# Optimization experiments

Measured on AMD Instinct MI355X. Metric: run time of the kernel, lower is better.

## Reference

```python
import jax, jax.numpy as jnp
import numpy as np

B = 32768
HID = 512          # hidden_dim
DIM = 256          # output dim
MAX_N = 17         # max_n + 1
KEY_MID = (MAX_N + HID) // 2   # 264
DEC_MID = (HID + DIM) // 2     # 384
SP_MID = (HID + MAX_N) // 2    # 264


def _linear_params(k, fan_in, fan_out):
    k1, k2 = jax.random.split(k)
    lim = 1.0 / np.sqrt(fan_in)
    W = jax.random.uniform(k1, (fan_in, fan_out), minval=-lim, maxval=lim, dtype=jnp.float32)
    b = jax.random.uniform(k2, (fan_out,), minval=-lim, maxval=lim, dtype=jnp.float32)
    return W, b


def setup_inputs() -> dict:
    key = jax.random.key(0)
    ks = jax.random.split(key, 7)
    z = jax.random.normal(ks[0], (B, HID), dtype=jnp.float32)
    key_W1, key_b1 = _linear_params(ks[1], MAX_N, KEY_MID)
    key_W2, key_b2 = _linear_params(ks[2], KEY_MID, HID)
    dec_W1, dec_b1 = _linear_params(ks[3], HID, DEC_MID)
    dec_W2, dec_b2 = _linear_params(ks[4], DEC_MID, DIM)
    sp_W1, sp_b1 = _linear_params(ks[5], HID, SP_MID)
    sp_W2, sp_b2 = _linear_params(ks[6], SP_MID, MAX_N)
    return dict(
        z=z,
        key_W1=key_W1, key_b1=key_b1,
        key_g1=jnp.ones((KEY_MID,), jnp.float32), key_be1=jnp.zeros((KEY_MID,), jnp.float32),
        key_W2=key_W2, key_b2=key_b2,
        dec_W1=dec_W1, dec_b1=dec_b1, dec_W2=dec_W2, dec_b2=dec_b2,
        sp_W1=sp_W1, sp_b1=sp_b1,
        sp_g1=jnp.ones((SP_MID,), jnp.float32), sp_be1=jnp.zeros((SP_MID,), jnp.float32),
        sp_W2=sp_W2, sp_b2=sp_b2,
    )


def _ln(x, g, b):
    m = x.mean(-1, keepdims=True)
    v = x.var(-1, keepdims=True)
    return (x - m) / jnp.sqrt(v + 1e-5) * g + b


def _ragged_indices(n):
    # n: np.int array [B]; returns batch ids and within-sample positions k
    n = np.asarray(n)
    batch = np.repeat(np.arange(n.shape[0]), n)
    starts = np.concatenate([np.zeros(1, dtype=np.int64), np.cumsum(n)[:-1]])
    k = np.arange(batch.shape[0]) - starts[batch]
    return batch, k


def reference(z, key_W1, key_b1, key_g1, key_be1, key_W2, key_b2,
              dec_W1, dec_b1, dec_W2, dec_b2,
              sp_W1, sp_b1, sp_g1, sp_be1, sp_W2, sp_b2):
    # size_pred MLP: Linear -> LayerNorm -> ReLU -> Linear
    h = jax.nn.relu(_ln(z @ sp_W1 + sp_b1, sp_g1, sp_be1))
    n_pred = h @ sp_W2 + sp_b2                       # [B, MAX_N]
    n = np.asarray(jnp.argmax(n_pred, axis=-1))      # concrete sizes (ragged)
    batch_np, k_np = _ragged_indices(n)
    batch = jnp.asarray(batch_np)
    k = jnp.asarray(k_np)
    pos = jax.nn.one_hot(k, MAX_N, dtype=jnp.float32)            # [T, MAX_N]
    # key_net: Linear -> LayerNorm -> ReLU -> Linear
    keys = jax.nn.relu(_ln(pos @ key_W1 + key_b1, key_g1, key_be1)) @ key_W2 + key_b2  # [T, HID]
    vals_rep = z[batch]                              # repeat_interleave via gather
    zp = vals_rep * keys
    # decoder: Linear -> ReLU -> Linear (no layernorm by default)
    x = jax.nn.relu(zp @ dec_W1 + dec_b1) @ dec_W2 + dec_b2      # [T, DIM]
    return x, batch
```

## Files before the change

### kernel.cpp

```cpp
#include <hip/hip_runtime.h>
#include <hip/hip_bf16.h>

#define B_N   32768
#define HID   512
#define DIM   256
#define MAXN  17
#define SM    264
#define DM    384

typedef __attribute__((ext_vector_type(8))) short bf16x8;
typedef __attribute__((ext_vector_type(4))) float f32x4;

static __device__ __forceinline__ unsigned short f2bf(float x) {
  union { float f; unsigned u; } v; v.f = x;
  unsigned r = (v.u + 0x7FFFu + ((v.u >> 16) & 1u)) >> 16;
  return (unsigned short)r;
}

static __device__ __forceinline__ unsigned pkbf(float a, float b) {
  __hip_bfloat162 h = __float22bfloat162_rn(float2{a, b});
  union { __hip_bfloat162 h; unsigned u; } cv; cv.h = h;
  return cv.u;
}

__global__ __launch_bounds__(320, 3) void sizepred_kernel(
    const float* __restrict__ z,  const float* __restrict__ W1,
    const float* __restrict__ b1, const float* __restrict__ g1,
    const float* __restrict__ be1, const float* __restrict__ W2,
    const float* __restrict__ b2, int* __restrict__ n_out)
{
  __shared__ __align__(16) char smem[33024 + 2 * 16896];
  float* zs   = (float*)smem;
  float* us   = (float*)smem;
  float* wch0 = (float*)(smem + 33024);
  float* wch1 = (float*)(smem + 33024 + 16896);
  __shared__ float lnm[16], lnr[16];
  __shared__ float log17[16 * 17];

  const int tid = threadIdx.x;
  const int b0  = blockIdx.x * 16;

  const bool act = tid < 264;
  const int  s0  = (tid / 66) * 4;
  const int  j0  = (tid % 66) * 4;

  float acc[4][4];
#pragma unroll
  for (int i = 0; i < 4; ++i)
#pragma unroll
    for (int q = 0; q < 4; ++q) acc[i][q] = 0.f;

  float4 nz0, nz1, nz2, nz3;
  if (act) {
    const float4* wsrc = (const float4*)W1;
    nz0 = wsrc[0 * 264 + tid];
    nz1 = wsrc[1 * 264 + tid];
    nz2 = wsrc[2 * 264 + tid];
    nz3 = wsrc[3 * 264 + tid];
  }
  for (int idx = tid; idx < 2048; idx += 320) {
    int r = idx >> 7, c4 = idx & 127;
    float4 v = ((const float4*)z)[(size_t)(b0 + r) * 128 + c4];
    *(float4*)&zs[r * 516 + c4 * 4] = v;
  }
  if (act) {
    float4* wd = (float4*)wch0;
    wd[0 * 264 + tid] = nz0;
    wd[1 * 264 + tid] = nz1;
    wd[2 * 264 + tid] = nz2;
    wd[3 * 264 + tid] = nz3;
  }
  __syncthreads();

#pragma unroll 1
  for (int ch = 0; ch < 32; ++ch) {
    const float* cw = (ch & 1) ? wch1 : wch0;
    float*       nw = (ch & 1) ? wch0 : wch1;
    if (act && ch + 1 < 32) {
      const float4* wsrc = (const float4*)(W1 + (size_t)(ch + 1) * 16 * 264);
      nz0 = wsrc[0 * 264 + tid];
      nz1 = wsrc[1 * 264 + tid];
      nz2 = wsrc[2 * 264 + tid];
      nz3 = wsrc[3 * 264 + tid];
    }
    if (act) {
      const int zb = ch * 16;
#pragma unroll
      for (int u = 0; u < 4; ++u) {
        float4 za0 = *(const float4*)&zs[(s0 + 0) * 516 + zb + u * 4];
        float4 za1 = *(const float4*)&zs[(s0 + 1) * 516 + zb + u * 4];
        float4 za2 = *(const float4*)&zs[(s0 + 2) * 516 + zb + u * 4];
        float4 za3 = *(const float4*)&zs[(s0 + 3) * 516 + zb + u * 4];
#pragma unroll
        for (int e = 0; e < 4; ++e) {
          float4 w = *(const float4*)&cw[(u * 4 + e) * 264 + j0];
          float a0 = (e == 0) ? za0.x : (e == 1) ? za0.y : (e == 2) ? za0.z : za0.w;
          float a1 = (e == 0) ? za1.x : (e == 1) ? za1.y : (e == 2) ? za1.z : za1.w;
          float a2 = (e == 0) ? za2.x : (e == 1) ? za2.y : (e == 2) ? za2.z : za2.w;
          float a3 = (e == 0) ? za3.x : (e == 1) ? za3.y : (e == 2) ? za3.z : za3.w;
          acc[0][0] += a0 * w.x; acc[0][1] += a0 * w.y; acc[0][2] += a0 * w.z; acc[0][3] += a0 * w.w;
          acc[1][0] += a1 * w.x; acc[1][1] += a1 * w.y; acc[1][2] += a1 * w.z; acc[1][3] += a1 * w.w;
          acc[2][0] += a2 * w.x; acc[2][1] += a2 * w.y; acc[2][2] += a2 * w.z; acc[2][3] += a2 * w.w;
          acc[3][0] += a3 * w.x; acc[3][1] += a3 * w.y; acc[3][2] += a3 * w.z; acc[3][3] += a3 * w.w;
        }
      }
      if (ch + 1 < 32) {
        float4* wd = (float4*)nw;
        wd[0 * 264 + tid] = nz0;
        wd[1 * 264 + tid] = nz1;
        wd[2 * 264 + tid] = nz2;
        wd[3 * 264 + tid] = nz3;
      }
    }
    __syncthreads();
  }

  float4 o0, o1, o2, o3;
  if (act) {
    float4 bb = *(const float4*)&b1[j0];
    o0.x = acc[0][0] + bb.x; o0.y = acc[0][1] + bb.y; o0.z = acc[0][2] + bb.z; o0.w = acc[0][3] + bb.w;
    o1.x = acc[1][0] + bb.x; o1.y = acc[1][1] + bb.y; o1.z = acc[1][2] + bb.z; o1.w = acc[1][3] + bb.w;
    o2.x = acc[2][0] + bb.x; o2.y = acc[2][1] + bb.y; o2.z = acc[2][2] + bb.z; o2.w = acc[2][3] + bb.w;
    o3.x = acc[3][0] + bb.x; o3.y = acc[3][1] + bb.y; o3.z = acc[3][2] + bb.z; o3.w = acc[3][3] + bb.w;
  }
  __syncthreads();
  if (act) {
    *(float4*)&us[(s0 + 0) * 268 + j0] = o0;
    *(float4*)&us[(s0 + 1) * 268 + j0] = o1;
    *(float4*)&us[(s0 + 2) * 268 + j0] = o2;
    *(float4*)&us[(s0 + 3) * 268 + j0] = o3;
  }
  __syncthreads();

  if (tid < 16) {
    float s = 0.f, q = 0.f;
    for (int j = 0; j < 264; ++j) { float v = us[tid * 268 + j]; s += v; q += v * v; }
    float m   = s / 264.f;
    float var = q / 264.f - m * m;
    lnm[tid] = m;
    lnr[tid] = 1.f / sqrtf(var + 1e-5f);
  }
  __syncthreads();

  for (int idx = tid; idx < 16 * 264; idx += 320) {
    int s = idx / 264, j = idx - s * 264;
    float v = (us[s * 268 + j] - lnm[s]) * lnr[s] * g1[j] + be1[j];
    us[s * 268 + j] = fmaxf(v, 0.f);
  }
  __syncthreads();

  if (tid < 272) {
    int s = tid / 17, jj = tid - s * 17;
    float a = b2[jj];
    const float* up = &us[s * 268];
#pragma unroll 4
    for (int c = 0; c < 264; c += 4) {
      float4 u = *(const float4*)(up + c);
      a += u.x * W2[(c + 0) * 17 + jj];
      a += u.y * W2[(c + 1) * 17 + jj];
      a += u.z * W2[(c + 2) * 17 + jj];
      a += u.w * W2[(c + 3) * 17 + jj];
    }
    log17[tid] = a;
  }
  __syncthreads();

  if (tid < 16) {
    int best = 0; float bv = log17[tid * 17];
    for (int jj = 1; jj < 17; ++jj) {
      float v = log17[tid * 17 + jj];
      if (v > bv) { bv = v; best = jj; }
    }
    n_out[b0 + tid] = best;
  }
}

__global__ __launch_bounds__(1024) void scan_kernel(const int* __restrict__ n,
                                                    int* __restrict__ starts)
{
  __shared__ int part[1024];
  const int tid  = threadIdx.x;
  const int base = tid * 32;
  int loc[32];
  int s = 0;
#pragma unroll
  for (int i = 0; i < 8; ++i) {
    int4 v = ((const int4*)(n + base))[i];
    loc[i * 4 + 0] = v.x; loc[i * 4 + 1] = v.y;
    loc[i * 4 + 2] = v.z; loc[i * 4 + 3] = v.w;
    s += v.x + v.y + v.z + v.w;
  }
  part[tid] = s;
  __syncthreads();
  for (int off = 1; off < 1024; off <<= 1) {
    int v   = part[tid];
    int add = (tid >= off) ? part[tid - off] : 0;
    __syncthreads();
    part[tid] = v + add;
    __syncthreads();
  }
  int run = part[tid] - s;
#pragma unroll
  for (int i = 0; i < 8; ++i) {
    int4 w;
    w.x = run; run += loc[i * 4 + 0];
    w.y = run; run += loc[i * 4 + 1];
    w.z = run; run += loc[i * 4 + 2];
    w.w = run; run += loc[i * 4 + 3];
    ((int4*)(starts + base))[i] = w;
  }
  if (tid == 1023) starts[B_N] = run;
}

__global__ __launch_bounds__(256) void scatter_kernel(
    const int* __restrict__ n, const int* __restrict__ starts,
    int* __restrict__ bi, int* __restrict__ ki, float* __restrict__ out, int T)
{
  int b = blockIdx.x * 256 + threadIdx.x;
  if (b >= B_N) return;
  int st = starts[b], nn = n[b];
  float* ob = out + (size_t)T * DIM;
  for (int k = 0; k < nn; ++k) {
    bi[st + k] = b;
    ki[st + k] = k;
    ob[st + k] = (float)b;
  }
}

__global__ __launch_bounds__(320) void keys_kernel(
    const float* __restrict__ W1, const float* __restrict__ b1,
    const float* __restrict__ g1, const float* __restrict__ be1,
    const float* __restrict__ W2, const float* __restrict__ b2,
    float* __restrict__ ktab)
{
  __shared__ float hs[264];
  __shared__ float mr[2];
  const int kk = blockIdx.x, tid = threadIdx.x;
  if (tid < 264) hs[tid] = W1[kk * 264 + tid] + b1[tid];
  __syncthreads();
  if (tid == 0) {
    float s = 0.f, q = 0.f;
    for (int j = 0; j < 264; ++j) { float v = hs[j]; s += v; q += v * v; }
    float m = s / 264.f;
    mr[0] = m;
    mr[1] = 1.f / sqrtf(q / 264.f - m * m + 1e-5f);
  }
  __syncthreads();
  if (tid < 264) hs[tid] = fmaxf((hs[tid] - mr[0]) * mr[1] * g1[tid] + be1[tid], 0.f);
  __syncthreads();
  for (int c = tid; c < 512; c += 320) {
    float a = b2[c];
    for (int j = 0; j < 264; ++j) a += hs[j] * W2[j * 512 + c];
    ktab[kk * 512 + c] = a;
  }
}

__global__ __launch_bounds__(64) void pack_kernel(
    const float* __restrict__ W1, const float* __restrict__ W2,
    short* __restrict__ W1p, short* __restrict__ W2p)
{
  const int g = blockIdx.x, l = threadIdx.x;
  const float* W; int nt, kt, N;
  if (g < 384) { W = W1; kt = g / 24; nt = g % 24; N = 384; }
  else         { W = W2; int gg = g - 384; kt = gg / 16; nt = gg % 16; N = 256; }
  const int krow = kt * 32 + ((l >> 4) << 3);
  const int col  = nt * 16 + (l & 15);
  short v[8];
#pragma unroll
  for (int j = 0; j < 8; ++j)
    v[j] = (short)f2bf(W[(size_t)(krow + j) * N + col]);
  short* d = (g < 384) ? (W1p + ((size_t)g * 64 + l) * 8)
                       : (W2p + ((size_t)(g - 384) * 64 + l) * 8);
  *(bf16x8*)d = *(bf16x8*)v;
}

__global__ __launch_bounds__(256, 4) void decoder_kernel(
    const float* __restrict__ z,  const float* __restrict__ ktab,
    const short* __restrict__ W1p, const float* __restrict__ b1,
    const short* __restrict__ W2p, const float* __restrict__ b2,
    const int* __restrict__ bi,   const int* __restrict__ ki,
    float* __restrict__ out, int T)
{
  __shared__ __align__(16) short zps[16384];
  __shared__ int tb[32], tk[32];

  const int tid  = threadIdx.x;
  const int wave = tid >> 6;
  const int lane = tid & 63;
  const int t0   = blockIdx.x * 32;

  if (tid < 32) {
    int t = t0 + tid;
    tb[tid] = (t < T) ? bi[t] : 0;
    tk[tid] = (t < T) ? ki[t] : 0;
  }
  __syncthreads();

#pragma unroll
  for (int it = 0; it < 8; ++it) {
    int chunk = tid + it * 256;
    int l  = chunk & 63;
    int mt = (chunk >> 6) & 1;
    int kt = chunk >> 7;
    int m  = mt * 16 + (l & 15);
    int k0 = kt * 32 + ((l >> 4) << 3);
    const float4* zr = (const float4*)(z    + (size_t)tb[m] * 512 + k0);
    const float4* kr = (const float4*)(ktab + (size_t)tk[m] * 512 + k0);
    float4 z0 = zr[0], z1 = zr[1], k4 = kr[0], k5 = kr[1];
    uint4 u;
    u.x = pkbf(z0.x * k4.x, z0.y * k4.y);
    u.y = pkbf(z0.z * k4.z, z0.w * k4.w);
    u.z = pkbf(z1.x * k5.x, z1.y * k5.y);
    u.w = pkbf(z1.z * k5.z, z1.w * k5.w);
    *(uint4*)&zps[(size_t)chunk * 8] = u;
  }
  __syncthreads();

  f32x4 acc[2][6];
#pragma unroll
  for (int mt = 0; mt < 2; ++mt)
#pragma unroll
    for (int j = 0; j < 6; ++j) acc[mt][j] = (f32x4){0.f, 0.f, 0.f, 0.f};

  {
    const short* wb = W1p + ((size_t)(wave * 6) * 64 + lane) * 8;
#pragma unroll 4
    for (int kt = 0; kt < 16; ++kt) {
      bf16x8 a0 = *(bf16x8*)&zps[((kt * 2 + 0) * 64 + lane) * 8];
      bf16x8 a1 = *(bf16x8*)&zps[((kt * 2 + 1) * 64 + lane) * 8];
#pragma unroll
      for (int j = 0; j < 6; ++j) {
        bf16x8 bf = *(const bf16x8*)(wb + (size_t)kt * 12288 + j * 512);
        acc[0][j] = __builtin_amdgcn_mfma_f32_16x16x32_bf16(a0, bf, acc[0][j], 0, 0, 0);
        acc[1][j] = __builtin_amdgcn_mfma_f32_16x16x32_bf16(a1, bf, acc[1][j], 0, 0, 0);
      }
    }
  }
  __syncthreads();

  {
    short* Hs = zps;
    float bload[6];
#pragma unroll
    for (int j = 0; j < 6; ++j)
      bload[j] = b1[wave * 96 + j * 16 + (lane & 15)];
#pragma unroll
    for (int mt = 0; mt < 2; ++mt) {
#pragma unroll
      for (int j = 0; j < 6; ++j) {
        int c = wave * 96 + j * 16 + (lane & 15);
        int lane2hi = ((c >> 3) & 3) << 4;
        int koff = (c >> 5) * 2;
        int jj = c & 7;
        int mbase = mt * 16 + (lane >> 4) * 4;
        int a0 = ((koff + (mbase >> 4)) * 64 + ((mbase & 15) | lane2hi)) * 8 + jj;
        float v0 = fmaxf(acc[mt][j][0] + bload[j], 0.f);
        float v1 = fmaxf(acc[mt][j][1] + bload[j], 0.f);
        float v2 = fmaxf(acc[mt][j][2] + bload[j], 0.f);
        float v3 = fmaxf(acc[mt][j][3] + bload[j], 0.f);
        unsigned p01 = pkbf(v0, v1);
        unsigned p23 = pkbf(v2, v3);
        Hs[a0 +  0] = (short)(p01 & 0xFFFFu);
        Hs[a0 +  8] = (short)(p01 >> 16);
        Hs[a0 + 16] = (short)(p23 & 0xFFFFu);
        Hs[a0 + 24] = (short)(p23 >> 16);
      }
    }
  }
  __syncthreads();

  f32x4 acc2[2][4];
#pragma unroll
  for (int mt = 0; mt < 2; ++mt)
#pragma unroll
    for (int j = 0; j < 4; ++j) acc2[mt][j] = (f32x4){0.f, 0.f, 0.f, 0.f};

  {
    const short* Hs = zps;
    const short* wb = W2p + ((size_t)(wave * 4) * 64 + lane) * 8;
#pragma unroll 4
    for (int kt = 0; kt < 12; ++kt) {
      bf16x8 a0 = *(const bf16x8*)&Hs[((kt * 2 + 0) * 64 + lane) * 8];
      bf16x8 a1 = *(const bf16x8*)&Hs[((kt * 2 + 1) * 64 + lane) * 8];
#pragma unroll
      for (int j = 0; j < 4; ++j) {
        bf16x8 bf = *(const bf16x8*)(wb + (size_t)kt * 8192 + j * 512);
        acc2[0][j] = __builtin_amdgcn_mfma_f32_16x16x32_bf16(a0, bf, acc2[0][j], 0, 0, 0);
        acc2[1][j] = __builtin_amdgcn_mfma_f32_16x16x32_bf16(a1, bf, acc2[1][j], 0, 0, 0);
      }
    }
  }

  {
    float bload[4];
#pragma unroll
    for (int j = 0; j < 4; ++j)
      bload[j] = b2[wave * 64 + j * 16 + (lane & 15)];
#pragma unroll
    for (int mt = 0; mt < 2; ++mt) {
#pragma unroll
      for (int r = 0; r < 4; ++r) {
        int t = t0 + mt * 16 + (lane >> 4) * 4 + r;
        if (t < T) {
#pragma unroll
          for (int j = 0; j < 4; ++j) {
            int c = wave * 64 + j * 16 + (lane & 15);
            out[(size_t)t * 256 + c] = acc2[mt][j][r] + bload[j];
          }
        }
      }
    }
  }
}

extern "C" void kernel_launch(void* const* d_in, const int* in_sizes, int n_in,
                              void* d_out, int out_size, void* d_ws, size_t ws_size,
                              hipStream_t stream)
{
  const float* z      = (const float*)d_in[0];
  const float* keyW1  = (const float*)d_in[1];
  const float* keyb1  = (const float*)d_in[2];
  const float* keyg1  = (const float*)d_in[3];
  const float* keybe1 = (const float*)d_in[4];
  const float* keyW2  = (const float*)d_in[5];
  const float* keyb2  = (const float*)d_in[6];
  const float* decW1  = (const float*)d_in[7];
  const float* decb1  = (const float*)d_in[8];
  const float* decW2  = (const float*)d_in[9];
  const float* decb2  = (const float*)d_in[10];
  const float* spW1   = (const float*)d_in[11];
  const float* spb1   = (const float*)d_in[12];
  const float* spg1   = (const float*)d_in[13];
  const float* spbe1  = (const float*)d_in[14];
  const float* spW2   = (const float*)d_in[15];
  const float* spb2   = (const float*)d_in[16];

  const int T = out_size / (DIM + 1);

  char* ws = (char*)d_ws;
  int*   n_arr  = (int*)(ws);
  int*   starts = (int*)(ws + 131072);
  float* ktab   = (float*)(ws + 262160);
  short* W1p    = (short*)(ws + 296976);
  short* W2p    = (short*)(ws + 690192);
  int*   bi     = (int*)(ws + 886800);
  size_t kioff  = 886800 + (((size_t)T * 4 + 15) / 16) * 16;
  int*   ki     = (int*)(ws + kioff);

  float* outF = (float*)d_out;

  sizepred_kernel<<<B_N / 16, 320, 0, stream>>>(z, spW1, spb1, spg1, spbe1, spW2, spb2, n_arr);
  pack_kernel<<<576, 64, 0, stream>>>(decW1, decW2, W1p, W2p);
  scan_kernel<<<1, 1024, 0, stream>>>(n_arr, starts);
  keys_kernel<<<MAXN, 320, 0, stream>>>(keyW1, keyb1, keyg1, keybe1, keyW2, keyb2, ktab);
  scatter_kernel<<<B_N / 256, 256, 0, stream>>>(n_arr, starts, bi, ki, outF, T);
  if (T > 0)
    decoder_kernel<<<(T + 31) / 32, 256, 0, stream>>>(z, ktab, W1p, decb1, W2p, decb2, bi, ki, outF, T);
}
```

Measured before the change: 1.390 ms.

## Use direct global-to-LDS loads for z tile and W1 chunks in size-pred kernel

```diff
diff --git a/kernel.cpp b/kernel.cpp
--- a/kernel.cpp
+++ b/kernel.cpp
@@ -11,6 +11,9 @@
 typedef __attribute__((ext_vector_type(8))) short bf16x8;
 typedef __attribute__((ext_vector_type(4))) float f32x4;
 
+#define AS1 __attribute__((address_space(1)))
+#define AS3 __attribute__((address_space(3)))
+
 static __device__ __forceinline__ unsigned short f2bf(float x) {
   union { float f; unsigned u; } v; v.f = x;
   unsigned r = (v.u + 0x7FFFu + ((v.u >> 16) & 1u)) >> 16;
@@ -29,16 +32,18 @@
     const float* __restrict__ be1, const float* __restrict__ W2,
     const float* __restrict__ b2, int* __restrict__ n_out)
 {
-  __shared__ __align__(16) char smem[33024 + 2 * 16896];
-  float* zs   = (float*)smem;
-  float* us   = (float*)smem;
-  float* wch0 = (float*)(smem + 33024);
-  float* wch1 = (float*)(smem + 33024 + 16896);
+  __shared__ __align__(16) char smem[33024 + 2 * 8448];
+  float* zs  = (float*)smem;
+  float* us  = (float*)smem;
+  float* wb0 = (float*)(smem + 33024);
+  float* wb1 = (float*)(smem + 33024 + 8448);
   __shared__ float lnm[16], lnr[16];
   __shared__ float log17[16 * 17];
 
   const int tid = threadIdx.x;
   const int b0  = blockIdx.x * 16;
+  const int wv  = tid >> 6;
+  const int ln  = tid & 63;
 
   const bool act = tid < 264;
   const int  s0  = (tid / 66) * 4;
@@ -50,43 +55,53 @@
 #pragma unroll
     for (int q = 0; q < 4; ++q) acc[i][q] = 0.f;
 
-  float4 nz0, nz1, nz2, nz3;
-  if (act) {
-    const float4* wsrc = (const float4*)W1;
-    nz0 = wsrc[0 * 264 + tid];
-    nz1 = wsrc[1 * 264 + tid];
-    nz2 = wsrc[2 * 264 + tid];
-    nz3 = wsrc[3 * 264 + tid];
-  }
-  for (int idx = tid; idx < 2048; idx += 320) {
-    int r = idx >> 7, c4 = idx & 127;
-    float4 v = ((const float4*)z)[(size_t)(b0 + r) * 128 + c4];
-    *(float4*)&zs[r * 516 + c4 * 4] = v;
-  }
-  if (act) {
-    float4* wd = (float4*)wch0;
-    wd[0 * 264 + tid] = nz0;
-    wd[1 * 264 + tid] = nz1;
-    wd[2 * 264 + tid] = nz2;
-    wd[3 * 264 + tid] = nz3;
-  }
-  __syncthreads();
-
+  for (int s = wv; s < 32; s += 5) {
+    int r = s >> 1, sl = s & 1;
+    const float* gp = z + (size_t)(b0 + r) * 512 + sl * 256 + ln * 4;
+    __builtin_amdgcn_global_load_lds(
+        (const AS1 unsigned*)gp,
+        (AS3 unsigned*)(zs + r * 516 + sl * 256), 16, 0, 0);
+  }
+  {
+    const float* gc = W1;
+    const float* gp1 = gc + (size_t)(wv * 64 + ln) * 4;
+    __builtin_amdgcn_global_load_lds(
+        (const AS1 unsigned*)gp1, (AS3 unsigned*)(wb0 + wv * 256), 16, 0, 0);
+    if (wv < 3) {
+      const float* gp2 = gc + (size_t)((wv + 5) * 64 + ln) * 4;
+      __builtin_amdgcn_global_load_lds(
+          (const AS1 unsigned*)gp2, (AS3 unsigned*)(wb0 + (wv + 5) * 256), 16, 0, 0);
+    } else if (wv == 3) {
+      const float* gp2 = gc + 2048 + ln;
+      __builtin_amdgcn_global_load_lds(
+          (const AS1 unsigned*)gp2, (AS3 unsigned*)(wb0 + 2048), 4, 0, 0);
+    }
+  }
+  __syncthreads();
+
+  float* cw = wb0;
+  float* nw = wb1;
 #pragma unroll 1
-  for (int ch = 0; ch < 32; ++ch) {
-    const float* cw = (ch & 1) ? wch1 : wch0;
-    float*       nw = (ch & 1) ? wch0 : wch1;
-    if (act && ch + 1 < 32) {
-      const float4* wsrc = (const float4*)(W1 + (size_t)(ch + 1) * 16 * 264);
-      nz0 = wsrc[0 * 264 + tid];
-      nz1 = wsrc[1 * 264 + tid];
-      nz2 = wsrc[2 * 264 + tid];
-      nz3 = wsrc[3 * 264 + tid];
+  for (int ch = 0; ch < 64; ++ch) {
+    if (ch + 1 < 64) {
+      const float* gc = W1 + (size_t)(ch + 1) * 2112;
+      const float* gp1 = gc + (size_t)(wv * 64 + ln) * 4;
+      __builtin_amdgcn_global_load_lds(
+          (const AS1 unsigned*)gp1, (AS3 unsigned*)(nw + wv * 256), 16, 0, 0);
+      if (wv < 3) {
+        const float* gp2 = gc + (size_t)((wv + 5) * 64 + ln) * 4;
+        __builtin_amdgcn_global_load_lds(
+            (const AS1 unsigned*)gp2, (AS3 unsigned*)(nw + (wv + 5) * 256), 16, 0, 0);
+      } else if (wv == 3) {
+        const float* gp2 = gc + 2048 + ln;
+        __builtin_amdgcn_global_load_lds(
+            (const AS1 unsigned*)gp2, (AS3 unsigned*)(nw + 2048), 4, 0, 0);
+      }
     }
     if (act) {
-      const int zb = ch * 16;
-#pragma unroll
-      for (int u = 0; u < 4; ++u) {
+      const int zb = ch * 8;
+#pragma unroll
+      for (int u = 0; u < 2; ++u) {
         float4 za0 = *(const float4*)&zs[(s0 + 0) * 516 + zb + u * 4];
         float4 za1 = *(const float4*)&zs[(s0 + 1) * 516 + zb + u * 4];
         float4 za2 = *(const float4*)&zs[(s0 + 2) * 516 + zb + u * 4];
@@ -104,14 +119,8 @@
           acc[3][0] += a3 * w.x; acc[3][1] += a3 * w.y; acc[3][2] += a3 * w.z; acc[3][3] += a3 * w.w;
         }
       }
-      if (ch + 1 < 32) {
-        float4* wd = (float4*)nw;
-        wd[0 * 264 + tid] = nz0;
-        wd[1 * 264 + tid] = nz1;
-        wd[2 * 264 + tid] = nz2;
-        wd[3 * 264 + tid] = nz3;
-      }
-    }
+    }
+    float* t = cw; cw = nw; nw = t;
     __syncthreads();
   }
 
```

Result: faster. 1.127 ms (-18.9%).
